# Kernel tuning notes

Measured on AMD Instinct MI355X. Metric: run time of the kernel, lower is better.

The kernel has to match this reference:

```python
import jax, jax.numpy as jnp
import numpy as np

B, H, W = 4, 256, 256
TARGET_BETA0 = 5
TARGET_LIFETIME = 0.5
LOSS_SCALE = 100.0


def setup_inputs() -> dict:
    key = jax.random.key(0)
    k1, k2 = jax.random.split(key)
    prob_map = jax.random.uniform(k1, (B, 1, H, W), dtype=jnp.float32)
    roi_mask = (jax.random.uniform(k2, (B, 1, H, W)) < 0.9).astype(jnp.float32)
    return {"prob_map": prob_map, "roi_mask": roi_mask}


def _ph0_topk_loss(f):
    """0-dim persistent homology (V-filtration, 4-connectivity) of f:[H,W],
    then standard top-k MSE(target_lifetime) loss. Equivalent to
    cripser.compute_ph_torch(f, maxdim=0, filtration='V') + _standard_loss.
    Algorithm: Kruskal over grid edges with weight max(f[u],f[v]), elder rule.
    All combinatorics run on stop_gradient values; births/deaths are
    differentiable gathers from f at the paired pixel indices."""
    Hh, Ww = f.shape
    N = Hh * Ww
    fv = f.reshape(-1)
    fvc = jax.lax.stop_gradient(fv)

    idx2d = jnp.arange(N, dtype=jnp.int32).reshape(Hh, Ww)
    r_u = idx2d[:, :-1].reshape(-1)  # right edges
    r_v = r_u + 1
    d_u = idx2d[:-1, :].reshape(-1)  # down edges
    d_v = d_u + Ww
    eu = jnp.concatenate([r_u, d_u])
    ev = jnp.concatenate([r_v, d_v])
    ew = jnp.maximum(fvc[eu], fvc[ev])
    order = jnp.argsort(ew)  # process edges by increasing filtration value
    eu, ev = eu[order], ev[order]

    parent0 = jnp.arange(N, dtype=jnp.int32)

    def step(parent, uv):
        u, v = uv[0], uv[1]

        def find(x):
            return jax.lax.while_loop(lambda y: parent[y] != y, lambda y: parent[y], x)

        ru = find(u)
        rv = find(v)
        merge = ru != rv
        # Invariant: a root is the argmin pixel of its component, so
        # fvc[root] is the component's birth value. Elder rule: the root
        # with smaller birth value survives (ties -> smaller index).
        older_u = (fvc[ru] < fvc[rv]) | ((fvc[ru] == fvc[rv]) & (ru < rv))
        keep = jnp.where(older_u, ru, rv)
        die = jnp.where(older_u, rv, ru)
        b_idx = jnp.where(merge, die, -1)  # birth pixel of the dying comp
        d_pix = jnp.where(fvc[u] >= fvc[v], u, v)  # death = max endpoint
        d_idx = jnp.where(merge, d_pix, -1)
        parent = parent.at[die].set(jnp.where(merge, keep, die))
        parent = parent.at[u].set(jnp.where(merge, keep, ru))  # path compression
        parent = parent.at[v].set(jnp.where(merge, keep, rv))
        return parent, (b_idx, d_idx)

    _, (pb, pd_) = jax.lax.scan(step, parent0, jnp.stack([eu, ev], axis=1))

    valid = pb >= 0
    births = fv[jnp.maximum(pb, 0)]
    deaths = fv[jnp.maximum(pd_, 0)]
    life = jnp.where(valid, deaths - births, 0.0)  # lifetimes >= 0

    # sort descending; invalid slots to the end (keys are stop-gradient)
    key_ = jnp.where(valid, jax.lax.stop_gradient(life), -jnp.inf)
    top = jnp.argsort(-key_)[:TARGET_BETA0]
    topk = life[top]
    vk = valid[top]
    n_use = jnp.sum(vk)  # = min(num_finite, target_beta0)
    sq = jnp.where(vk, (topk - TARGET_LIFETIME) ** 2, 0.0)
    return jnp.sum(sq) / jnp.maximum(n_use, 1).astype(f.dtype)


def reference(prob_map, roi_mask):
    prob = prob_map[:, 0] * roi_mask[:, 0]  # roi masking; (1-roi)*0 is a no-op
    filtration = 1.0 - prob
    losses = jax.vmap(_ph0_topk_loss)(filtration)
    return jnp.mean(losses) * LOSS_SCALE
```

## Files before the change

kernel.cpp:

```cpp
#include <hip/hip_runtime.h>
#include <stdint.h>

#define NPIX 65536
#define NRE  65280
#define NE   130560
#define NIMG 4
#define LTPB 1024
#define ETPB 1024
#define NBLK_L (NIMG*32)
#define TPIX 2048
#define EPAD 4096
#define KMAX 4096
#define HSZ  1024
#define LHSZ 2048
#define ECAP 4096
#define NCUT 2560
typedef unsigned long long u64;

__device__ __forceinline__ int ufind(unsigned* lbl, int x){
  int r = x, c = (int)lbl[r];
  while (c != r){ r = c; c = (int)lbl[r]; }
  while ((int)lbl[x] != r){ int n = (int)lbl[x]; lbl[x] = (unsigned)r; x = n; }
  return r;
}
__device__ __forceinline__ int ufind16(unsigned short* uf, int x){
  int r = x, c = (int)uf[r];
  while (c != r){ r = c; c = (int)uf[r]; }
  while ((int)uf[x] != r){ int n = (int)uf[x]; uf[x] = (unsigned short)r; x = n; }
  return r;
}
__device__ __forceinline__ void uflat(unsigned* lbl, int x){
  int r = (int)lbl[x];
  if (r == x) return;
  int c = (int)lbl[r];
  while (c != r){ r = c; c = (int)lbl[r]; }
  lbl[x] = (unsigned)r;
}
__device__ __forceinline__ void uflat16(unsigned short* uf, int x){
  int r = (int)uf[x];
  if (r == x) return;
  int c = (int)uf[r];
  while (c != r){ r = c; c = (int)uf[r]; }
  uf[x] = (unsigned short)r;
}

__device__ __forceinline__ void merge5(float* a, const float* b){
  float out[5]; int ia = 0, ib = 0;
  #pragma unroll
  for (int k = 0; k < 5; ++k){
    float av = (ia < 5) ? a[ia] : -2.0f;
    float bv = (ib < 5) ? b[ib] : -2.0f;
    if (av >= bv){ out[k] = av; ++ia; } else { out[k] = bv; ++ib; }
  }
  #pragma unroll
  for (int k = 0; k < 5; ++k) a[k] = out[k];
}

__device__ __forceinline__ void ins5(float* t5, float v){
  if (v > t5[4]){
    int j = 4;
    while (j > 0 && t5[j-1] < v){ t5[j] = t5[j-1]; --j; }
    t5[j] = v;
  }
}

__global__ __launch_bounds__(LTPB)
void ph0_local(const float* __restrict__ prob, const float* __restrict__ roi,
               float* __restrict__ LIFEg, unsigned* __restrict__ CIDg,
               u64* __restrict__ LAg,
               unsigned* __restrict__ C, unsigned* __restrict__ C2,
               unsigned* __restrict__ CUTWg, u64* __restrict__ RNKIg,
               float* __restrict__ T5g)
{
  const int blk = blockIdx.x;
  const int img = blk >> 5;
  const int tile = blk & 31;
  const int tr = tile >> 2, tc = tile & 3;
  const int gr0 = tr*32, gc0 = tc*64;
  const int tid = threadIdx.x;
  const int lane = tid & 63;

  const float* pm = prob + img*NPIX;
  const float* rm = roi  + img*NPIX;
  float* LIFE = LIFEg + img*NPIX;
  unsigned* CID = CIDg + img*NPIX;
  unsigned* CUTW = CUTWg + img*NCUT;
  u64* RNKI = RNKIg + (size_t)img*NPIX;
  u64* LA = LAg + (size_t)img*NE;

  __shared__ float          sf[TPIX];
  __shared__ unsigned       slbl[TPIX];
  __shared__ unsigned       smeb[2][TPIX];
  __shared__ float          slife[TPIX];
  __shared__ unsigned short el[2][EPAD];
  __shared__ unsigned       aux[EPAD];
  __shared__ unsigned       bkw[192];
  __shared__ unsigned short bkp[192];
  __shared__ unsigned       s_fired[TPIX/32];
  __shared__ float          s_t5w[(LTPB/64)*5];
  __shared__ int s_n[3];

  float t5[5] = {-1.f,-1.f,-1.f,-1.f,-1.f};

  for (int p = tid; p < TPIX; p += LTPB){
    int gp = ((gr0 + (p>>6))<<8) + gc0 + (p&63);
    float fv = 1.0f - pm[gp]*rm[gp];
    sf[p] = fv; slbl[p] = (unsigned)p;
    smeb[0][p] = 0xFFFFFFFFu; smeb[1][p] = 0xFFFFFFFFu;
    slife[p] = 0.0f;
  }
  if (tid < 3) s_n[tid] = 0;
  if (tid < TPIX/32) s_fired[tid] = 0;
  for (int s = tid; s < 192; s += LTPB){
    unsigned wv = 0xFFFFFFFFu; int p = 0; int gq = -1;
    if (s < 32){ if (tc > 0){ p = s*64;        gq = ((gr0+s)<<8)    + gc0 - 1;  } }
    else if (s < 64){ int k=s-32;  if (tc < 3){ p = k*64+63;  gq = ((gr0+k)<<8)  + gc0 + 64; } }
    else if (s < 128){ int k=s-64; if (tr > 0){ p = k;        gq = ((gr0-1)<<8)  + gc0 + k;  } }
    else { int k=s-128;            if (tr < 7){ p = 31*64+k;  gq = ((gr0+32)<<8) + gc0 + k;  } }
    if (gq >= 0){
      int gp = ((gr0 + (p>>6))<<8) + gc0 + (p&63);
      float fp = 1.0f - pm[gp]*rm[gp];
      float fq = 1.0f - pm[gq]*rm[gq];
      wv = __float_as_uint(fmaxf(fp, fq));
    }
    bkw[s] = wv; bkp[s] = (unsigned short)p;
  }
  __syncthreads();

  if (tid < 192){
    int s = tid;
    if (s >= 32 && s < 64  && tc < 3) CUTW[(tc<<8) | (gr0 + (s-32))] = bkw[s];
    if (s >= 128           && tr < 7) CUTW[768 + (tr<<8) + (gc0 + (s-128))] = bkw[s];
  }

  int M = EPAD, cur = 0;
  for (int rd = 0; rd < 100000; ++rd){
    int nxt = cur ^ 1;
    unsigned* sme = smeb[rd & 1];
    int bs = tid - (LTPB - 192);
    if (bs >= 0){
      unsigned wv = bkw[bs];
      if (wv != 0xFFFFFFFFu) atomicMin(&sme[ufind(slbl, (int)bkp[bs])], wv);
    }
    int Mpad = (M + 63) & ~63;
    for (int idx = tid; idx < Mpad; idx += LTPB){
      bool keep = false; int e=0,u=0,v=0,a=0,b=0;
      if (idx < M){
        e = (rd == 0) ? idx : (int)el[cur][idx];
        bool valid;
        if (e < 2048){ u=e; v=e+1; valid = ((e&63)!=63); }
        else { u=e-2048; v=u+64; valid = ((u>>6)!=31); }
        if (valid){
          a = ufind(slbl,u); b = ufind(slbl,v);
          if (a != b){
            unsigned wb = __float_as_uint(fmaxf(sf[u],sf[v]));
            atomicMin(&sme[a],wb); atomicMin(&sme[b],wb);
            keep = true;
          }
        }
      }
      u64 m = __ballot(keep);
      if (m){
        int pos0 = __popcll(m & ((1ULL<<lane)-1));
        int leader = __ffsll((long long)m)-1;
        int base = 0;
        if (lane == leader) base = atomicAdd(&s_n[rd%3], __popcll(m));
        base = __shfl(base, leader);
        if (keep){
          el[nxt][base+pos0] = (unsigned short)e;
          aux[base+pos0] = (unsigned)a | ((unsigned)b<<16);
        }
      }
    }
    __syncthreads();
    int n = s_n[rd%3];
    cur = nxt;
    if (n == M || n == 0){ M = n; break; }
    M = n;
    for (int idx = tid; idx < M; idx += LTPB){
      int e = (int)el[cur][idx];
      unsigned ab = aux[idx];
      int a = (int)(ab & 0xFFFFu), b = (int)(ab >> 16);
      int u, v;
      if (e < 2048){ u = e; v = e + 1; } else { u = e - 2048; v = u + 64; }
      float w = fmaxf(sf[u], sf[v]);
      unsigned wb = __float_as_uint(w);
      float fa = sf[a], fb = sf[b];
      bool bd = (fb < fa) || ((fb == fa) && (b < a));
      int die = bd ? a : b, keep = bd ? b : a;
      if (sme[die] == wb){
        slbl[die] = (unsigned)keep;
        float lt = w - (bd ? fa : fb);
        slife[die] = lt;
        unsigned bbit = 1u << (die & 31);
        if (!(atomicOr(&s_fired[die >> 5], bbit) & bbit)) ins5(t5, lt);
      }
    }
    for (int p = tid; p < TPIX; p += LTPB) uflat(slbl, p);
    {
      unsigned* smeN = smeb[(rd+1) & 1];
      for (int i = tid; i < TPIX; i += LTPB) smeN[i] = 0xFFFFFFFFu;
      if (tid == 0) s_n[(rd+1)%3] = 0;
    }
    __syncthreads();
  }

  unsigned* posm = smeb[0];
  for (int p = tid; p < TPIX; p += LTPB){
    if ((int)slbl[p] == p){
      unsigned pos = atomicAdd(&C2[img], 1u);
      posm[p] = pos;
      unsigned gp = (unsigned)(((gr0 + (p>>6))<<8) + gc0 + (p&63));
      RNKI[pos] = ((u64)__float_as_uint(sf[p]) << 32) | gp;
    }
  }
  __syncthreads();
  for (int p = tid; p < TPIX; p += LTPB){
    int r = ufind(slbl, p);
    int gp = ((gr0 + (p>>6))<<8) + gc0 + (p&63);
    CID[gp] = posm[r];
    LIFE[gp] = slife[p];
  }
  __syncthreads();

  unsigned* hk = (unsigned*)&el[cur ^ 1][0];
  unsigned* hw = slbl;
  for (int i = tid; i < LHSZ; i += LTPB){ hk[i] = 0xFFFFFFFFu; hw[i] = 0xFFFFFFFFu; }
  __syncthreads();

  unsigned* ctr = &C[img];
  int Mpad2 = (M + 63) & ~63;
  for (int idx = tid; idx < Mpad2; idx += LTPB){
    bool spill = false;
    u64 rec = 0;
    if (idx < M){
      int e = (int)el[cur][idx];
      unsigned ab = aux[idx];
      int a = (int)(ab & 0xFFFFu), b = (int)(ab >> 16);
      int u, v;
      if (e < 2048){ u = e; v = e + 1; } else { u = e - 2048; v = u + 64; }
      unsigned wb = __float_as_uint(fmaxf(sf[u], sf[v]));
      int lo = a < b ? a : b, hi = a < b ? b : a;
      unsigned key = ((unsigned)lo << 11) | (unsigned)hi;
      unsigned h = ((key * 2654435761u) >> 21) & (LHSZ-1);
      bool ins = false;
      #pragma unroll
      for (int t = 0; t < 8; ++t){
        unsigned old = atomicCAS(&hk[h], 0xFFFFFFFFu, key);
        if (old == 0xFFFFFFFFu || old == key){ atomicMin(&hw[h], wb); ins = true; break; }
        h = (h + 1) & (LHSZ-1);
      }
      if (!ins){
        spill = true;
        rec = ((u64)wb << 32) | ((u64)posm[a] << 16) | posm[b];
      }
    }
    u64 m = __ballot(spill);
    if (m){
      int pos0 = __popcll(m & ((1ULL<<lane)-1));
      int leader = __ffsll((long long)m)-1;
      unsigned base = 0;
      if (lane == leader) base = atomicAdd(ctr, (unsigned)__popcll(m));
      base = (unsigned)__shfl((int)base, leader);
      if (spill) LA[base + pos0] = rec;
    }
  }
  __syncthreads();
  for (int h = tid; h < LHSZ; h += LTPB){
    unsigned key = hk[h];
    bool ok = (key != 0xFFFFFFFFu);
    u64 rec = 0;
    if (ok){
      int a = (int)(key >> 11), b = (int)(key & 0x7FFu);
      rec = ((u64)hw[h] << 32) | ((u64)posm[a] << 16) | posm[b];
    }
    u64 m = __ballot(ok);
    if (m){
      int pos0 = __popcll(m & ((1ULL<<lane)-1));
      int leader = __ffsll((long long)m)-1;
      unsigned base = 0;
      if (lane == leader) base = atomicAdd(ctr, (unsigned)__popcll(m));
      base = (unsigned)__shfl((int)base, leader);
      if (ok) LA[base + pos0] = rec;
    }
  }

  #pragma unroll
  for (int off = 1; off < 64; off <<= 1){
    float o[5];
    #pragma unroll
    for (int k = 0; k < 5; ++k) o[k] = __shfl_xor(t5[k], off);
    merge5(t5, o);
  }
  if (lane == 0){
    int wv = tid >> 6;
    #pragma unroll
    for (int k = 0; k < 5; ++k) s_t5w[wv*5+k] = t5[k];
  }
  __syncthreads();
  if (tid < 64){
    float u5[5];
    #pragma unroll
    for (int k = 0; k < 5; ++k) u5[k] = (tid < LTPB/64) ? s_t5w[tid*5+k] : -2.0f;
    #pragma unroll
    for (int off = 1; off < 16; off <<= 1){
      float o[5];
      #pragma unroll
      for (int k = 0; k < 5; ++k) o[k] = __shfl_xor(u5[k], off);
      merge5(u5, o);
    }
    if (tid == 0){
      #pragma unroll
      for (int k = 0; k < 5; ++k) T5g[blk*5+k] = u5[k];
    }
  }
}

#define RUN_ROUNDS_GLOBAL(UF, ME, RNK)                                       \
  for (int k = tid; k < K; k += ETPB) UF[k] = (unsigned short)k;             \
  __syncthreads();                                                           \
  for (int rd = 0; rd < 70000 && n > 0; ++rd){                               \
    for (int k = tid; k < K; k += ETPB) ME[k] = 0xFFFFFFFFu;                 \
    if (tid == 0) s_n[0] = 0;                                                \
    __syncthreads();                                                         \
    int Mpad = (n + 63) & ~63;                                               \
    for (int idx = tid; idx < Mpad; idx += ETPB){                            \
      bool keep = false; unsigned wb = 0; int a = 0, b = 0;                  \
      if (idx < n){                                                          \
        u64 rec = src[idx];                                                  \
        wb = (unsigned)(rec >> 32);                                          \
        a = (int)((rec >> 16) & 0xFFFFu);                                    \
        b = (int)(rec & 0xFFFFu);                                            \
        a = ufind16(UF, a); b = ufind16(UF, b);                              \
        if (a != b){ atomicMin(&ME[a], wb); atomicMin(&ME[b], wb); keep = true; } \
      }                                                                      \
      u64 m = __ballot(keep);                                                \
      if (m){                                                                \
        int pos0 = __popcll(m & ((1ULL<<lane)-1));                           \
        int leader = __ffsll((long long)m)-1;                                \
        int base = 0;                                                        \
        if (lane == leader) base = atomicAdd(&s_n[0], __popcll(m));          \
        base = __shfl(base, leader);                                         \
        if (keep) dst[base+pos0] = ((u64)wb<<32)|((u64)(unsigned)a<<16)|(unsigned)b; \
      }                                                                      \
    }                                                                        \
    __syncthreads();                                                         \
    int nn = s_n[0];                                                         \
    for (int idx = tid; idx < nn; idx += ETPB){                              \
      u64 rec = dst[idx];                                                    \
      unsigned wb = (unsigned)(rec >> 32);                                   \
      int a = (int)((rec >> 16) & 0xFFFFu);                                  \
      int b = (int)(rec & 0xFFFFu);                                          \
      bool bd = RNK[b] < RNK[a];                                             \
      int die = bd ? a : b, kp = bd ? b : a;                                 \
      if (ME[die] == wb){                                                    \
        UF[die] = (unsigned short)kp;                                        \
        u64 rk = RNK[die];                                                   \
        life[(unsigned)(rk & 0xFFFFFFFFu)] =                                 \
            __uint_as_float(wb) - __uint_as_float((unsigned)(rk >> 32));     \
      }                                                                      \
    }                                                                        \
    __syncthreads();                                                         \
    u64* t = src; src = dst; dst = t; n = nn;                                \
  }

__global__ __launch_bounds__(ETPB)
void ph0_endgame(float* __restrict__ LIFEg, unsigned* __restrict__ CIDg,
                 const unsigned* __restrict__ CUTWg, u64* __restrict__ RNKIg,
                 u64* __restrict__ LAg, u64* __restrict__ LBg,
                 const unsigned* __restrict__ C, const unsigned* __restrict__ C2,
                 const float* __restrict__ T5g,
                 float* __restrict__ LOSS, unsigned* __restrict__ DONE,
                 float* __restrict__ out)
{
  const int img = blockIdx.x, tid = threadIdx.x;
  const int lane = tid & 63;
  float* life = LIFEg + img*NPIX;
  unsigned* cid = CIDg + img*NPIX;
  const unsigned* cw = CUTWg + img*NCUT;
  u64* RNKI = RNKIg + (size_t)img*NPIX;
  u64* src = LAg + (size_t)img*NE;
  u64* dst = LBg + (size_t)img*NE;

  __shared__ unsigned short s_uf[KMAX];
  __shared__ unsigned s_meB[2*KMAX];
  __shared__ unsigned s_hkB[2*HSZ];
  __shared__ unsigned s_hwB[2*HSZ];
  __shared__ u64 s_rnk[KMAX];
  __shared__ u64 s_lstA[ECAP];
  __shared__ u64 s_lstB[ECAP];
  __shared__ unsigned s_fired[KMAX/32];
  __shared__ float s_w5[(ETPB/64)*5];
  __shared__ int s_n[3];

  const int K = (int)C2[img];
  const int nInt = (int)C[img];

  for (int s = tid; s < NCUT; s += ETPB){
    int gu, gv;
    if (s < 768){ int ci = s >> 8, row = s & 255, col = 63 + (ci<<6); gu = (row<<8)+col; gv = gu+1; }
    else { int k = s - 768; int ri = k >> 8, colh = k & 255, gr = 31 + (ri<<5); gu = (gr<<8)+colh; gv = gu+256; }
    unsigned ia = cid[gu];
    unsigned ib = cid[gv];
    unsigned wb = cw[s];
    s_lstA[s] = ((u64)wb << 32) | ((u64)ia << 16) | ib;
  }
  if (tid < 3) s_n[tid] = 0;
  int n = nInt + NCUT;

  float t5[5] = {-1.f,-1.f,-1.f,-1.f,-1.f};

  if (K <= KMAX){
    for (int k = tid; k < K; k += ETPB){
      s_uf[k] = (unsigned short)k;
      s_rnk[k] = RNKI[k];
      s_meB[k] = 0xFFFFFFFFu;
    }
    for (int h = tid; h < HSZ; h += ETPB){ s_hkB[h] = 0xFFFFFFFFu; s_hwB[h] = 0xFFFFFFFFu; }
    if (tid < KMAX/32) s_fired[tid] = 0;
    if (tid < 32*5) ins5(t5, T5g[img*(32*5) + tid]);
    __syncthreads();

    u64 *lsrc = s_lstA, *ldst = s_lstB;

    for (int rd = 0; rd < 70000; ++rd){
      const int bi = rd & 1;
      unsigned* me = s_meB + bi*KMAX;
      unsigned* hk = s_hkB + bi*HSZ;
      unsigned* hw = s_hwB + bi*HSZ;
      const bool useHash = (n > 1024);
      int Mpad = (n + 63) & ~63;
      for (int idx = tid; idx < Mpad; idx += ETPB){
        bool app = false; unsigned wb = 0; int a = 0, b = 0;
        if (idx < n){
          u64 rec;
          if (rd == 0) rec = (idx < NCUT) ? lsrc[idx] : src[idx - NCUT];
          else         rec = (idx < ECAP) ? lsrc[idx] : src[idx];
          a = (int)((rec >> 16) & 0xFFFFu);
          b = (int)(rec & 0xFFFFu);
          a = ufind16(s_uf, a); b = ufind16(s_uf, b);
          if (a != b){
            wb = (unsigned)(rec >> 32);
            if (useHash){
              int lo = a < b ? a : b, hi = a < b ? b : a;
              unsigned key = ((unsigned)lo << 12) | (unsigned)hi;
              unsigned h = ((key * 2654435761u) >> 20) & (HSZ-1);
              bool ins = false;
              #pragma unroll
              for (int t = 0; t < 8; ++t){
                unsigned old = atomicCAS(&hk[h], 0xFFFFFFFFu, key);
                if (old == 0xFFFFFFFFu || old == key){ atomicMin(&hw[h], wb); ins = true; break; }
                h = (h + 1) & (HSZ-1);
              }
              if (!ins){ atomicMin(&me[a], wb); atomicMin(&me[b], wb); app = true; }
            } else {
              atomicMin(&me[a], wb); atomicMin(&me[b], wb); app = true;
            }
          }
        }
        u64 m = __ballot(app);
        if (m){
          int pos0 = __popcll(m & ((1ULL<<lane)-1));
          int leader = __ffsll((long long)m)-1;
          int base = 0;
          if (lane == leader) base = atomicAdd(&s_n[rd%3], __popcll(m));
          base = __shfl(base, leader);
          if (app){
            u64 r = ((u64)wb<<32)|((u64)(unsigned)a<<16)|(unsigned)b;
            int pos = base+pos0;
            if (pos < ECAP) ldst[pos] = r; else dst[pos] = r;
          }
        }
      }
      __syncthreads();
      if (useHash){
        for (int h = tid; h < HSZ; h += ETPB){
          unsigned key = hk[h];
          bool okk = (key != 0xFFFFFFFFu);
          unsigned wb = 0; int a = 0, b = 0;
          if (okk){
            a = (int)(key >> 12); b = (int)(key & 0xFFFu);
            wb = hw[h];
            atomicMin(&me[a], wb); atomicMin(&me[b], wb);
          }
          u64 m = __ballot(okk);
          if (m){
            int pos0 = __popcll(m & ((1ULL<<lane)-1));
            int leader = __ffsll((long long)m)-1;
            int base = 0;
            if (lane == leader) base = atomicAdd(&s_n[rd%3], __popcll(m));
            base = __shfl(base, leader);
            if (okk){
              u64 r = ((u64)wb<<32)|((u64)(unsigned)a<<16)|(unsigned)b;
              int pos = base+pos0;
              if (pos < ECAP) ldst[pos] = r; else dst[pos] = r;
            }
          }
        }
        __syncthreads();
      }
      int nn = s_n[rd%3];
      if (nn == 0) break;
      for (int idx = tid; idx < nn; idx += ETPB){
        u64 rec = (idx < ECAP) ? ldst[idx] : dst[idx];
        unsigned wb = (unsigned)(rec >> 32);
        int a = (int)((rec >> 16) & 0xFFFFu);
        int b = (int)(rec & 0xFFFFu);
        u64 ra = s_rnk[a], rb = s_rnk[b];
        bool bd = rb < ra;
        int die = bd ? a : b, kp = bd ? b : a;
        if (me[die] == wb){
          s_uf[die] = (unsigned short)kp;
          unsigned bbit = 1u << (die & 31);
          if (!(atomicOr(&s_fired[die >> 5], bbit) & bbit)){
            u64 rk = bd ? ra : rb;
            ins5(t5, __uint_as_float(wb) - __uint_as_float((unsigned)(rk >> 32)));
          }
        }
      }
      for (int k = tid; k < K; k += ETPB) uflat16(s_uf, k);
      {
        unsigned* meN = s_meB + (bi^1)*KMAX;
        for (int k = tid; k < K; k += ETPB) meN[k] = 0xFFFFFFFFu;
        if (nn > 1024){
          unsigned* hkN = s_hkB + (bi^1)*HSZ;
          unsigned* hwN = s_hwB + (bi^1)*HSZ;
          for (int h = tid; h < HSZ; h += ETPB){ hkN[h] = 0xFFFFFFFFu; hwN[h] = 0xFFFFFFFFu; }
        }
        if (tid == 0) s_n[(rd+1)%3] = 0;
      }
      __syncthreads();
      { u64* t = src; src = dst; dst = t; }
      { u64* t = lsrc; lsrc = ldst; ldst = t; }
      n = nn;
    }
  } else {
    __syncthreads();
    for (int s = tid; s < NCUT; s += ETPB) src[nInt + s] = s_lstA[s];
    __syncthreads();
    unsigned short* g_uf = (unsigned short*)cid;
    unsigned*       g_me = (unsigned*)(cid + NPIX/2);
    u64*            g_rnk = RNKI;
    RUN_ROUNDS_GLOBAL(g_uf, g_me, g_rnk)
    for (int i = tid; i < NPIX; i += ETPB) ins5(t5, life[i]);
  }

  #pragma unroll
  for (int off = 1; off < 64; off <<= 1){
    float o[5];
    #pragma unroll
    for (int k = 0; k < 5; ++k) o[k] = __shfl_xor(t5[k], off);
    merge5(t5, o);
  }
  if (lane == 0){
    int wv = tid >> 6;
    #pragma unroll
    for (int k = 0; k < 5; ++k) s_w5[wv*5+k] = t5[k];
  }
  __syncthreads();
  if (tid < 64){
    float u5[5];
    #pragma unroll
    for (int k = 0; k < 5; ++k) u5[k] = (tid < ETPB/64) ? s_w5[tid*5+k] : -2.0f;
    #pragma unroll
    for (int off = 1; off < 16; off <<= 1){
      float o[5];
      #pragma unroll
      for (int k = 0; k < 5; ++k) o[k] = __shfl_xor(u5[k], off);
      merge5(u5, o);
    }
    if (tid == 0){
      float lsum = 0.0f;
      #pragma unroll
      for (int k = 0; k < 5; ++k){ float d = u5[k] - 0.5f; lsum += d*d; }
      atomicExch(&LOSS[img], lsum * 0.2f);
      __threadfence();
      unsigned prev = atomicAdd(DONE, 1u);
      if (prev == NIMG - 1){
        float s = 0.0f;
        #pragma unroll
        for (int i = 0; i < NIMG; ++i) s += atomicAdd(&LOSS[i], 0.0f);
        out[0] = s * 25.0f;
      }
    }
  }
}

extern "C" void kernel_launch(void* const* d_in, const int* in_sizes, int n_in,
                              void* d_out, int out_size, void* d_ws, size_t ws_size,
                              hipStream_t stream)
{
  const float* prob = (const float*)d_in[0];
  const float* roi  = (const float*)d_in[1];
  char* ws = (char*)d_ws;
  const size_t SZL = (size_t)4*NE*8;
  float*    LIFE = (float*)(ws + (1u<<20));
  unsigned* CID  = (unsigned*)(ws + (2u<<20));
  unsigned* CUTW = (unsigned*)(ws + (3u<<20));
  u64*      LA   = (u64*)(ws + (5u<<20));
  u64*      LB   = (u64*)(ws + (5u<<20) + SZL);
  u64*      RNKI = (u64*)(ws + (5u<<20) + 2*SZL);
  unsigned* C    = (unsigned*)(ws + (5u<<20) + 2*SZL + (2u<<20));
  unsigned* C2   = C + 4;
  unsigned* DONE = C + 8;
  float*    LOSS = (float*)((char*)C + 64);
  float*    T5   = (float*)(ws + (5u<<20) + 2*SZL - 2560);
  float*    out  = (float*)d_out;

  hipMemsetAsync(C, 0, 64, stream);
  ph0_local<<<NBLK_L, LTPB, 0, stream>>>(prob, roi, LIFE, CID, LA, C, C2, CUTW, RNKI, T5);
  ph0_endgame<<<NIMG, ETPB, 0, stream>>>(LIFE, CID, CUTW, RNKI, LA, LB, C, C2, T5, LOSS, DONE, out);
}
```

Baseline: 262.4 us.

## Switch Boruvka rounds to single-wave tail and drop per-round flatten/reset sweeps

Both the local-tile and per-image Boruvka loops now hand off to a single 64-lane wavefront once the active edge list gets small. From then on, rounds run with wave barriers instead of block-wide __syncthreads. The full-array union-find flatten pass and the full min-edge array reset each round are removed. Instead, only the entries touched by surviving edges are reset for the next round. This cuts per-round barrier and sweep overhead in the long tail of rounds, at the cost of serialising the remaining work on one wave and relying on path compression inside find.

```diff
diff --git a/kernel.cpp b/kernel.cpp
--- a/kernel.cpp
+++ b/kernel.cpp
@@ -15,6 +15,8 @@
 #define LHSZ 2048
 #define ECAP 4096
 #define NCUT 2560
+#define MTAILL 256
+#define ETAIL  256
 typedef unsigned long long u64;
 
 __device__ __forceinline__ int ufind(unsigned* lbl, int x){
@@ -28,20 +30,6 @@
   while (c != r){ r = c; c = (int)uf[r]; }
   while ((int)uf[x] != r){ int n = (int)uf[x]; uf[x] = (unsigned short)r; x = n; }
   return r;
-}
-__device__ __forceinline__ void uflat(unsigned* lbl, int x){
-  int r = (int)lbl[x];
-  if (r == x) return;
-  int c = (int)lbl[r];
-  while (c != r){ r = c; c = (int)lbl[r]; }
-  lbl[x] = (unsigned)r;
-}
-__device__ __forceinline__ void uflat16(unsigned short* uf, int x){
-  int r = (int)uf[x];
-  if (r == x) return;
-  int c = (int)uf[r];
-  while (c != r){ r = c; c = (int)uf[r]; }
-  uf[x] = (unsigned short)r;
 }
 
 __device__ __forceinline__ void merge5(float* a, const float* b){
@@ -133,10 +121,12 @@
     if (s >= 128           && tr < 7) CUTW[768 + (tr<<8) + (gc0 + (s-128))] = bkw[s];
   }
 
-  int M = EPAD, cur = 0;
-  for (int rd = 0; rd < 100000; ++rd){
+  int M = EPAD, cur = 0, rd = 0;
+  bool tailm = false;
+  for (; rd < 100000; ++rd){
     int nxt = cur ^ 1;
-    unsigned* sme = smeb[rd & 1];
+    unsigned* sme  = smeb[rd & 1];
+    unsigned* smeN = smeb[(rd+1) & 1];
     int bs = tid - (LTPB - 192);
     if (bs >= 0){
       unsigned wv = bkw[bs];
@@ -195,14 +185,81 @@
         unsigned bbit = 1u << (die & 31);
         if (!(atomicOr(&s_fired[die >> 5], bbit) & bbit)) ins5(t5, lt);
       }
-    }
-    for (int p = tid; p < TPIX; p += LTPB) uflat(slbl, p);
-    {
-      unsigned* smeN = smeb[(rd+1) & 1];
-      for (int i = tid; i < TPIX; i += LTPB) smeN[i] = 0xFFFFFFFFu;
-      if (tid == 0) s_n[(rd+1)%3] = 0;
-    }
+      smeN[a] = 0xFFFFFFFFu; smeN[b] = 0xFFFFFFFFu;
+    }
+    if (tid == 0) s_n[(rd+1)%3] = 0;
     __syncthreads();
+    if (M <= MTAILL){ ++rd; tailm = true; break; }
+  }
+
+  if (tailm){
+    if (tid < 64){
+      for (;; ++rd){
+        unsigned* sme  = smeb[rd & 1];
+        unsigned* smeN = smeb[(rd+1) & 1];
+        for (int s = lane; s < 192; s += 64){
+          unsigned wv = bkw[s];
+          if (wv != 0xFFFFFFFFu) atomicMin(&sme[ufind(slbl, (int)bkp[s])], wv);
+        }
+        __builtin_amdgcn_wave_barrier();
+        int nxt = cur ^ 1;
+        int nacc = 0;
+        for (int i0 = 0; i0 < M; i0 += 64){
+          int idx = i0 + lane;
+          bool keep = false; int e = 0, a = 0, b = 0;
+          if (idx < M){
+            e = (int)el[cur][idx];
+            int u, v;
+            if (e < 2048){ u = e; v = e + 1; } else { u = e - 2048; v = u + 64; }
+            a = ufind(slbl,u); b = ufind(slbl,v);
+            if (a != b){
+              unsigned wb = __float_as_uint(fmaxf(sf[u],sf[v]));
+              atomicMin(&sme[a],wb); atomicMin(&sme[b],wb);
+              keep = true;
+            }
+          }
+          u64 mm = __ballot(keep);
+          if (keep){
+            int pos = nacc + __popcll(mm & ((1ULL<<lane)-1));
+            el[nxt][pos] = (unsigned short)e;
+            aux[pos] = (unsigned)a | ((unsigned)b<<16);
+          }
+          nacc += __popcll(mm);
+        }
+        __builtin_amdgcn_wave_barrier();
+        int n = nacc;
+        cur = nxt;
+        if (n == M || n == 0){ M = n; break; }
+        M = n;
+        for (int i0 = 0; i0 < M; i0 += 64){
+          int idx = i0 + lane;
+          if (idx < M){
+            int e = (int)el[cur][idx];
+            unsigned ab = aux[idx];
+            int a = (int)(ab & 0xFFFFu), b = (int)(ab >> 16);
+            int u, v;
+            if (e < 2048){ u = e; v = e + 1; } else { u = e - 2048; v = u + 64; }
+            float w = fmaxf(sf[u], sf[v]);
+            unsigned wb = __float_as_uint(w);
+            float fa = sf[a], fb = sf[b];
+            bool bd = (fb < fa) || ((fb == fa) && (b < a));
+            int die = bd ? a : b, kp = bd ? b : a;
+            if (sme[die] == wb){
+              slbl[die] = (unsigned)kp;
+              float lt = w - (bd ? fa : fb);
+              slife[die] = lt;
+              unsigned bbit = 1u << (die & 31);
+              if (!(atomicOr(&s_fired[die >> 5], bbit) & bbit)) ins5(t5, lt);
+            }
+            smeN[a] = 0xFFFFFFFFu; smeN[b] = 0xFFFFFFFFu;
+          }
+        }
+        __builtin_amdgcn_wave_barrier();
+      }
+      if (lane == 0){ s_n[0] = M; s_n[1] = cur; }
+    }
+    __syncthreads();
+    M = s_n[0]; cur = s_n[1];
   }
 
   unsigned* posm = smeb[0];
@@ -319,7 +376,7 @@
 #define RUN_ROUNDS_GLOBAL(UF, ME, RNK)                                       \
   for (int k = tid; k < K; k += ETPB) UF[k] = (unsigned short)k;             \
   __syncthreads();                                                           \
-  for (int rd = 0; rd < 70000 && n > 0; ++rd){                               \
+  for (int rdg = 0; rdg < 70000 && n > 0; ++rdg){                            \
     for (int k = tid; k < K; k += ETPB) ME[k] = 0xFFFFFFFFu;                 \
     if (tid == 0) s_n[0] = 0;                                                \
     __syncthreads();                                                         \
@@ -422,10 +479,12 @@
     __syncthreads();
 
     u64 *lsrc = s_lstA, *ldst = s_lstB;
-
-    for (int rd = 0; rd < 70000; ++rd){
+    int rd = 0; bool tailm = false;
+
+    for (; rd < 70000; ++rd){
       const int bi = rd & 1;
-      unsigned* me = s_meB + bi*KMAX;
+      unsigned* me  = s_meB + bi*KMAX;
+      unsigned* meN = s_meB + (bi^1)*KMAX;
       unsigned* hk = s_hkB + bi*HSZ;
       unsigned* hw = s_hwB + bi*HSZ;
       const bool useHash = (n > 1024);
@@ -517,22 +576,79 @@
             ins5(t5, __uint_as_float(wb) - __uint_as_float((unsigned)(rk >> 32)));
           }
         }
-      }
-      for (int k = tid; k < K; k += ETPB) uflat16(s_uf, k);
-      {
-        unsigned* meN = s_meB + (bi^1)*KMAX;
-        for (int k = tid; k < K; k += ETPB) meN[k] = 0xFFFFFFFFu;
-        if (nn > 1024){
-          unsigned* hkN = s_hkB + (bi^1)*HSZ;
-          unsigned* hwN = s_hwB + (bi^1)*HSZ;
-          for (int h = tid; h < HSZ; h += ETPB){ hkN[h] = 0xFFFFFFFFu; hwN[h] = 0xFFFFFFFFu; }
-        }
-        if (tid == 0) s_n[(rd+1)%3] = 0;
-      }
+        meN[a] = 0xFFFFFFFFu; meN[b] = 0xFFFFFFFFu;
+      }
+      if (nn > 1024){
+        unsigned* hkN = s_hkB + (bi^1)*HSZ;
+        unsigned* hwN = s_hwB + (bi^1)*HSZ;
+        for (int h = tid; h < HSZ; h += ETPB){ hkN[h] = 0xFFFFFFFFu; hwN[h] = 0xFFFFFFFFu; }
+      }
+      if (tid == 0) s_n[(rd+1)%3] = 0;
       __syncthreads();
       { u64* t = src; src = dst; dst = t; }
-      { u64* t = lsrc; lsrc = ldst; ldst = t; }
+      { u64* t2 = lsrc; lsrc = ldst; ldst = t2; }
       n = nn;
+      if (n <= ETAIL){ ++rd; tailm = true; break; }
+    }
+
+    if (tailm){
+      if (tid < 64){
+        for (;; ++rd){
+          const int bi = rd & 1;
+          unsigned* me  = s_meB + bi*KMAX;
+          unsigned* meN = s_meB + (bi^1)*KMAX;
+          int nacc = 0;
+          for (int i0 = 0; i0 < n; i0 += 64){
+            int idx = i0 + lane;
+            bool app = false; unsigned wb = 0; int a = 0, b = 0;
+            if (idx < n){
+              u64 rec = lsrc[idx];
+              a = (int)((rec >> 16) & 0xFFFFu);
+              b = (int)(rec & 0xFFFFu);
+              a = ufind16(s_uf, a); b = ufind16(s_uf, b);
+              if (a != b){
+                wb = (unsigned)(rec >> 32);
+                atomicMin(&me[a], wb); atomicMin(&me[b], wb);
+                app = true;
+              }
+            }
+            u64 mm = __ballot(app);
+            if (app){
+              int pos = nacc + __popcll(mm & ((1ULL<<lane)-1));
+              ldst[pos] = ((u64)wb<<32)|((u64)(unsigned)a<<16)|(unsigned)b;
+            }
+            nacc += __popcll(mm);
+          }
+          __builtin_amdgcn_wave_barrier();
+          int nn = nacc;
+          if (nn == 0) break;
+          for (int i0 = 0; i0 < nn; i0 += 64){
+            int idx = i0 + lane;
+            if (idx < nn){
+              u64 rec = ldst[idx];
+              unsigned wb = (unsigned)(rec >> 32);
+              int a = (int)((rec >> 16) & 0xFFFFu);
+              int b = (int)(rec & 0xFFFFu);
+              u64 ra = s_rnk[a], rb = s_rnk[b];
+              bool bd = rb < ra;
+              int die = bd ? a : b, kp = bd ? b : a;
+              if (me[die] == wb){
+                s_uf[die] = (unsigned short)kp;
+                unsigned bbit = 1u << (die & 31);
+                if (!(atomicOr(&s_fired[die >> 5], bbit) & bbit)){
+                  u64 rk = bd ? ra : rb;
+                  ins5(t5, __uint_as_float(wb) - __uint_as_float((unsigned)(rk >> 32)));
+                }
+              }
+              meN[a] = 0xFFFFFFFFu; meN[b] = 0xFFFFFFFFu;
+            }
+          }
+          __builtin_amdgcn_wave_barrier();
+          { u64* t2 = lsrc; lsrc = ldst; ldst = t2; }
+          n = nn;
+        }
+      }
+      __syncthreads();
     }
   } else {
     __syncthreads();
```

New measurement: 258.7 us. About the same (-1.4%).
